# Optimization experiments

Measured on AMD Instinct MI355X. Metric: run time of the kernel, lower is better.

Reference implementation:

```python
import math
import jax, jax.numpy as jnp
import numpy as np

PROB_SPARSE_FACTOR = 0.4


def setup_inputs() -> dict:
    key = jax.random.key(0)
    kq, kk, kv = jax.random.split(key, 3)
    B, H, T, S, D = 2, 16, 2048, 2048, 64
    q = jax.random.normal(kq, (B, H, T, D), dtype=jnp.float32)
    k = jax.random.normal(kk, (B, H, S, D), dtype=jnp.float32)
    v = jax.random.normal(kv, (B, H, S, D), dtype=jnp.float32)
    return {"q": q, "k": k, "v": v}


def reference(q, k, v):
    B, H, T, D = q.shape
    S = k.shape[2]
    scaling = 1.0 / math.sqrt(D)
    # Informer-style top-u query count (static, derived from shapes)
    u = max(int(min(PROB_SPARSE_FACTOR * math.log(S), T * 0.5)), int(T * 0.3))

    # KLD scoring over full attention approximation: [B,H,T,S]
    attn_approx = jnp.einsum("bhtd,bhsd->bhts", q * scaling, k)
    attn_approx = jnp.clip(attn_approx, -50.0, 50.0)
    attn_approx = attn_approx - jnp.max(attn_approx, axis=-1, keepdims=True)
    sm = jax.nn.softmax(attn_approx, axis=-1)
    log_uniform = math.log(S)
    kl_score = jnp.sum(sm * (jnp.log(sm + 1e-10) + log_uniform), axis=-1)  # [B,H,T]

    # Select top-u most informative queries per (b,h)
    _, topk_idx = jax.lax.top_k(kl_score, u)  # [B,H,u]

    # Sparse attention only for selected queries
    q_red = jnp.take_along_axis(q, topk_idx[..., None], axis=2)  # [B,H,u,D]
    scores = jnp.einsum("bhud,bhsd->bhus", q_red, k) * scaling
    scores = jnp.clip(scores, -50.0, 50.0)
    scores = scores - jnp.max(scores, axis=-1, keepdims=True)
    w = jax.nn.softmax(scores, axis=-1)
    w = jnp.clip(w, 1e-9, 1.0)
    out_red = jnp.einsum("bhus,bhsd->bhud", w, v)  # [B,H,u,D]

    # Scatter reduced outputs back into a zero-initialized full output
    b_i = jnp.arange(B)[:, None, None]
    h_i = jnp.arange(H)[None, :, None]
    out = jnp.zeros_like(q).at[b_i, h_i, topk_idx].set(out_red)
    return out
```

## Files before the change

### kernel.cpp

```cpp
#include <hip/hip_runtime.h>
#include <math.h>

#define T_DIM 2048
#define S_DIM 2048
#define D_DIM 64
#define BH_DIM 32
#define U_SEL 614
#define LOG_S_D 7.624618986159398
#define LOG2E_F 1.4426950408889634f
#define LN2_D 0.6931471805599453
#define SCL_Q (0.125f * LOG2E_F)

typedef __attribute__((ext_vector_type(8))) short bf16x8;
typedef __attribute__((ext_vector_type(4))) short bf16x4;
typedef __attribute__((ext_vector_type(4))) float f32x4;

__device__ __forceinline__ unsigned short bf16_rne(float x) {
  unsigned u = __float_as_uint(x);
  u += 0x7FFF + ((u >> 16) & 1);
  return (unsigned short)(u >> 16);
}
__device__ __forceinline__ float bf16_to_f(unsigned short h) {
  return __uint_as_float(((unsigned)h) << 16);
}

#define GLD_LDS16(g, l)                                                        \
  __builtin_amdgcn_global_load_lds(                                            \
      (const __attribute__((address_space(1))) unsigned int*)(const void*)(g), \
      (__attribute__((address_space(3))) unsigned int*)(void*)(l), 16, 0, 0)

__device__ __forceinline__ void stage_img(const unsigned short* __restrict__ g,
                                          unsigned short* l, int lane, int w) {
#pragma unroll
  for (int it = 0; it < 4; ++it) {
    const int chunk = it * 4 + w;
    GLD_LDS16((const char*)g + chunk * 1024 + lane * 16, (char*)l + chunk * 1024);
  }
}

__device__ __forceinline__ bf16x8 ldfrag_sw(const unsigned short* buf, int row, int chunk) {
  return *(const bf16x8*)(buf + (row << 6) + (((chunk) ^ (row & 7)) << 3));
}

__global__ __launch_bounds__(256) void convert_kernel(
    const float* __restrict__ kin, const float* __restrict__ vin,
    unsigned short* __restrict__ khi_g, unsigned short* __restrict__ klo_g,
    unsigned short* __restrict__ vt_g, float* __restrict__ out) {
  __shared__ float vld[128][65];
  const int jb = blockIdx.x;
  const int tid = threadIdx.x;
  if (jb < 512) {
    const int bh = jb >> 4, tl = jb & 15;
    const float* src = kin + ((size_t)bh * 2048 + tl * 128) * 64;
    unsigned short* dhi = khi_g + (size_t)(bh * 16 + tl) * 8192;
    unsigned short* dlo = klo_g + (size_t)(bh * 16 + tl) * 8192;
#pragma unroll
    for (int g = 0; g < 4; ++g) {
      const int flat = g * 256 + tid;
      const int r = flat >> 3, c = flat & 7;
      const float4 f0 = *(const float4*)(src + r * 64 + c * 8);
      const float4 f1 = *(const float4*)(src + r * 64 + c * 8 + 4);
      const float xs[8] = {f0.x, f0.y, f0.z, f0.w, f1.x, f1.y, f1.z, f1.w};
      bf16x8 hv, lv;
#pragma unroll
      for (int j = 0; j < 8; ++j) {
        const unsigned short h = bf16_rne(xs[j]);
        hv[j] = (short)h;
        lv[j] = (short)bf16_rne(xs[j] - bf16_to_f(h));
      }
      const int base = (r << 6) + ((c ^ (r & 7)) << 3);
      *(bf16x8*)(dhi + base) = hv;
      *(bf16x8*)(dlo + base) = lv;
    }
  } else if (jb < 1024) {
    const int jv = jb - 512;
    const int bh = jv >> 4, tl = jv & 15;
    const float* src = vin + ((size_t)bh * 2048 + tl * 128) * 64;
#pragma unroll
    for (int g = 0; g < 8; ++g) {
      const int f = g * 256 + tid;
      const int r = f >> 4, c4 = f & 15;
      const float4 x = *(const float4*)(src + r * 64 + c4 * 4);
      vld[r][c4 * 4 + 0] = x.x;
      vld[r][c4 * 4 + 1] = x.y;
      vld[r][c4 * 4 + 2] = x.z;
      vld[r][c4 * 4 + 3] = x.w;
    }
    __syncthreads();
    unsigned short* dst = vt_g + (size_t)(bh * 16 + tl) * 8192;
#pragma unroll
    for (int g = 0; g < 4; ++g) {
      const int oc = g * 256 + tid;
      const int d = oc >> 4, cc = oc & 15;
      bf16x8 hv;
#pragma unroll
      for (int j = 0; j < 8; ++j) hv[j] = (short)bf16_rne(vld[cc * 8 + j][d]);
      *(bf16x8*)(dst + (d << 7) + (((cc ^ (d & 15))) << 3)) = hv;
    }
  } else {
    float4* o4 = (float4*)out;
    const size_t b = (size_t)(jb - 1024);
#pragma unroll
    for (int g = 0; g < 8; ++g)
      o4[b * 2048 + g * 256 + tid] = make_float4(0.f, 0.f, 0.f, 0.f);
  }
}

__global__ __launch_bounds__(256, 2) void kl_score_mfma(
    const float* __restrict__ q, const unsigned short* __restrict__ khi_g,
    const unsigned short* __restrict__ klo_g, float* __restrict__ klout) {
  __shared__ __align__(16) unsigned short lds[2][16384];
  const int bh = blockIdx.y;
  const int t0 = blockIdx.x * 128;
  const int tid = threadIdx.x;
  const int lane = tid & 63, w = tid >> 6, quad = lane >> 4, l15 = lane & 15;
  const float* qb = q + (size_t)bh * (2048 * 64) + (size_t)t0 * 64;
  const unsigned short* khb = khi_g + (size_t)bh * 16 * 8192;
  const unsigned short* klb = klo_g + (size_t)bh * 16 * 8192;

  {
    unsigned short* qhi = &lds[1][0];
    unsigned short* qlo = &lds[1][8192];
#pragma unroll
    for (int g = 0; g < 4; ++g) {
      const int flat = g * 256 + tid;
      const int r = flat >> 3, c = flat & 7;
      const float4 f0 = *(const float4*)(qb + r * 64 + c * 8);
      const float4 f1 = *(const float4*)(qb + r * 64 + c * 8 + 4);
      const float xs[8] = {f0.x, f0.y, f0.z, f0.w, f1.x, f1.y, f1.z, f1.w};
      bf16x8 hv, lv;
#pragma unroll
      for (int j = 0; j < 8; ++j) {
        const float x = xs[j] * SCL_Q;
        const unsigned short h = bf16_rne(x);
        hv[j] = (short)h;
        lv[j] = (short)bf16_rne(x - bf16_to_f(h));
      }
      const int base = (r << 6) + ((c ^ (r & 7)) << 3);
      *(bf16x8*)(qhi + base) = hv;
      *(bf16x8*)(qlo + base) = lv;
    }
  }
  stage_img(khb, &lds[0][0], lane, w);
  stage_img(klb, &lds[0][8192], lane, w);
  __syncthreads();

  bf16x8 ah[2][2], al[2][2];
#pragma unroll
  for (int rt = 0; rt < 2; ++rt) {
    const int row = w * 32 + rt * 16 + l15;
#pragma unroll
    for (int kc = 0; kc < 2; ++kc) {
      ah[rt][kc] = ldfrag_sw(&lds[1][0], row, kc * 4 + quad);
      al[rt][kc] = ldfrag_sw(&lds[1][8192], row, kc * 4 + quad);
    }
  }
  __syncthreads();

  double Zd[8], Wd[8];
#pragma unroll
  for (int i = 0; i < 8; ++i) { Zd[i] = 0.0; Wd[i] = 0.0; }

  for (int st = 0; st < 16; ++st) {
    if (st < 15) {
      unsigned short* nb = &lds[(st + 1) & 1][0];
      stage_img(khb + (size_t)(st + 1) * 8192, nb, lane, w);
      stage_img(klb + (size_t)(st + 1) * 8192, nb + 8192, lane, w);
    }
    const unsigned short* cb = &lds[st & 1][0];

    f32x4 acc[2][8];
#pragma unroll
    for (int rt = 0; rt < 2; ++rt)
#pragma unroll
      for (int ct = 0; ct < 8; ++ct) acc[rt][ct] = (f32x4){0.f, 0.f, 0.f, 0.f};

#pragma unroll
    for (int ct = 0; ct < 8; ++ct) {
      const int srow = ct * 16 + l15;
      const bf16x8 bh0 = ldfrag_sw(cb, srow, quad);
      const bf16x8 bl0 = ldfrag_sw(cb + 8192, srow, quad);
      const bf16x8 bh1 = ldfrag_sw(cb, srow, 4 + quad);
      const bf16x8 bl1 = ldfrag_sw(cb + 8192, srow, 4 + quad);
#pragma unroll
      for (int rt = 0; rt < 2; ++rt) {
        f32x4 c = acc[rt][ct];
        c = __builtin_amdgcn_mfma_f32_16x16x32_bf16(ah[rt][0], bh0, c, 0, 0, 0);
        c = __builtin_amdgcn_mfma_f32_16x16x32_bf16(al[rt][0], bh0, c, 0, 0, 0);
        c = __builtin_amdgcn_mfma_f32_16x16x32_bf16(ah[rt][0], bl0, c, 0, 0, 0);
        c = __builtin_amdgcn_mfma_f32_16x16x32_bf16(ah[rt][1], bh1, c, 0, 0, 0);
        c = __builtin_amdgcn_mfma_f32_16x16x32_bf16(al[rt][1], bh1, c, 0, 0, 0);
        c = __builtin_amdgcn_mfma_f32_16x16x32_bf16(ah[rt][1], bl1, c, 0, 0, 0);
        acc[rt][ct] = c;
      }
    }

#pragma unroll
    for (int rt = 0; rt < 2; ++rt)
#pragma unroll
      for (int r = 0; r < 4; ++r) {
        float zp = 0.f, wp = 0.f;
#pragma unroll
        for (int ct = 0; ct < 8; ++ct) {
          const float t = acc[rt][ct][r];
          const float e = exp2f(t);
          zp += e;
          wp = fmaf(e, t, wp);
        }
        Zd[rt * 4 + r] += (double)zp;
        Wd[rt * 4 + r] += (double)wp;
      }
    __syncthreads();
  }

#pragma unroll
  for (int i = 0; i < 8; ++i) {
    double Zt = Zd[i], Wt = Wd[i];
#pragma unroll
    for (int mask = 1; mask <= 8; mask <<= 1) {
      Zt += __shfl_xor(Zt, mask);
      Wt += __shfl_xor(Wt, mask);
    }
    if (l15 == 0) {
      const double kl = LN2_D * (Wt / Zt) - log(Zt) + LOG_S_D;
      const int row = t0 + w * 32 + (i >> 2) * 16 + quad * 4 + (i & 3);
      klout[(size_t)bh * T_DIM + row] = (float)kl;
    }
  }
}

__global__ __launch_bounds__(1024) void topk_kernel(const float* __restrict__ kl,
                                                    int* __restrict__ topk) {
  __shared__ float sv[2048];
  __shared__ int si[2048];
  const int bh = blockIdx.x;
  const int tid = threadIdx.x;
  for (int i = tid; i < 2048; i += 1024) { sv[i] = kl[(size_t)bh * 2048 + i]; si[i] = i; }
  __syncthreads();
  for (int kk = 2; kk <= 2048; kk <<= 1) {
    for (int j = kk >> 1; j > 0; j >>= 1) {
      const int p = tid;
      const int i = ((p & ~(j - 1)) << 1) | (p & (j - 1));
      const int pr = i | j;
      const float v1 = sv[i], v2 = sv[pr];
      const int i1 = si[i], i2 = si[pr];
      const bool beforePI = (v2 > v1) || (v2 == v1 && i2 < i1);
      const bool dirDesc = ((i & kk) == 0);
      const bool doSwap = dirDesc ? beforePI : !beforePI;
      if (doSwap) { sv[i] = v2; sv[pr] = v1; si[i] = i2; si[pr] = i1; }
      __syncthreads();
    }
  }
  for (int i = tid; i < U_SEL; i += 1024) topk[bh * U_SEL + i] = si[i];
}

struct __align__(16) SmC {
  unsigned short qs[64 * 64];
  unsigned short kt[128 * 64];
  union { unsigned short vt[64 * 128]; float obuf[64 * 64]; } u;
  unsigned short ps[4][64 * 40];
  float zred[4][64];
};

__global__ __launch_bounds__(256, 2) void sparse_attn_mfma(
    const float* __restrict__ q, const unsigned short* __restrict__ khi_g,
    const unsigned short* __restrict__ vt_g, const int* __restrict__ topk,
    float* __restrict__ out) {
  __shared__ SmC sm;
  const int bh = blockIdx.y;
  const int l0 = blockIdx.x * 64;
  const int tid = threadIdx.x;
  const int lane = tid & 63, w = tid >> 6, quad = lane >> 4, l15 = lane & 15;
  const float* qb = q + (size_t)bh * (2048 * 64);
  const unsigned short* khb = khi_g + (size_t)bh * 16 * 8192;
  const unsigned short* vtb = vt_g + (size_t)bh * 16 * 8192;
  const int* tkb = topk + bh * U_SEL;

  {
#pragma unroll
    for (int g = 0; g < 2; ++g) {
      const int ch = g * 256 + tid;
      const int r = ch >> 3, c = ch & 7;
      const int l = l0 + r;
      const int row = (l < U_SEL) ? tkb[l] : tkb[0];
      const float4 f0 = *(const float4*)(qb + (size_t)row * 64 + c * 8);
      const float4 f1 = *(const float4*)(qb + (size_t)row * 64 + c * 8 + 4);
      const float xs[8] = {f0.x, f0.y, f0.z, f0.w, f1.x, f1.y, f1.z, f1.w};
      bf16x8 hv;
#pragma unroll
      for (int j = 0; j < 8; ++j) hv[j] = (short)bf16_rne(xs[j] * SCL_Q);
      *(bf16x8*)&sm.qs[(r << 6) + ((c ^ (r & 7)) << 3)] = hv;
    }
  }
  stage_img(khb, sm.kt, lane, w);
  stage_img(vtb, sm.u.vt, lane, w);
  __syncthreads();

  bf16x8 qf[4][2];
#pragma unroll
  for (int nt = 0; nt < 4; ++nt)
#pragma unroll
    for (int kc = 0; kc < 2; ++kc)
      qf[nt][kc] = ldfrag_sw(sm.qs, nt * 16 + l15, kc * 4 + quad);

  float zrun[4] = {0.f, 0.f, 0.f, 0.f};
  f32x4 oacc[4][4];
#pragma unroll
  for (int a = 0; a < 4; ++a)
#pragma unroll
    for (int b = 0; b < 4; ++b) oacc[a][b] = (f32x4){0.f, 0.f, 0.f, 0.f};

  for (int st = 0; st < 16; ++st) {
    f32x4 sacc[2][4];
#pragma unroll
    for (int mt = 0; mt < 2; ++mt)
#pragma unroll
      for (int nt = 0; nt < 4; ++nt) sacc[mt][nt] = (f32x4){0.f, 0.f, 0.f, 0.f};
#pragma unroll
    for (int mt = 0; mt < 2; ++mt) {
      const int arow = w * 32 + mt * 16 + l15;
      const bf16x8 a0 = ldfrag_sw(sm.kt, arow, quad);
      const bf16x8 a1 = ldfrag_sw(sm.kt, arow, 4 + quad);
#pragma unroll
      for (int nt = 0; nt < 4; ++nt) {
        f32x4 c = sacc[mt][nt];
        c = __builtin_amdgcn_mfma_f32_16x16x32_bf16(a0, qf[nt][0], c, 0, 0, 0);
        c = __builtin_amdgcn_mfma_f32_16x16x32_bf16(a1, qf[nt][1], c, 0, 0, 0);
        sacc[mt][nt] = c;
      }
    }

#pragma unroll
    for (int nt = 0; nt < 4; ++nt) {
      float zl = 0.f;
#pragma unroll
      for (int mt = 0; mt < 2; ++mt) {
        bf16x4 pw;
#pragma unroll
        for (int r = 0; r < 4; ++r) {
          const float p = exp2f(sacc[mt][nt][r]);
          zl += p;
          pw[r] = (short)bf16_rne(p);
        }
        *(bf16x4*)&sm.ps[w][(nt * 16 + l15) * 40 + mt * 16 + quad * 4] = pw;
      }
      zrun[nt] += zl;
    }

    {
      bf16x8 vbf[4];
#pragma unroll
      for (int dt = 0; dt < 4; ++dt) {
        const int d = dt * 16 + l15;
        vbf[dt] = *(const bf16x8*)&sm.u.vt[(d << 7) + (((w * 4 + quad) ^ l15) << 3)];
      }
#pragma unroll
      for (int mtq = 0; mtq < 4; ++mtq) {
        const bf16x8 pa = *(const bf16x8*)&sm.ps[w][(mtq * 16 + l15) * 40 + quad * 8];
#pragma unroll
        for (int dt = 0; dt < 4; ++dt)
          oacc[mtq][dt] = __builtin_amdgcn_mfma_f32_16x16x32_bf16(pa, vbf[dt], oacc[mtq][dt], 0, 0, 0);
      }
    }
    __syncthreads();
    if (st < 15) {
      stage_img(khb + (size_t)(st + 1) * 8192, sm.kt, lane, w);
      stage_img(vtb + (size_t)(st + 1) * 8192, sm.u.vt, lane, w);
      __syncthreads();
    }
  }

#pragma unroll
  for (int nt = 0; nt < 4; ++nt) {
    float z = zrun[nt];
    z += __shfl_xor(z, 16);
    z += __shfl_xor(z, 32);
    if (quad == 0) sm.zred[w][nt * 16 + l15] = z;
  }
  for (int i = tid; i < 64 * 64; i += 256) sm.u.obuf[i] = 0.f;
  __syncthreads();
#pragma unroll
  for (int mtq = 0; mtq < 4; ++mtq)
#pragma unroll
    for (int r = 0; r < 4; ++r) {
      const int qr = mtq * 16 + quad * 4 + r;
#pragma unroll
      for (int dt = 0; dt < 4; ++dt)
        atomicAdd(&sm.u.obuf[qr * 64 + dt * 16 + l15], oacc[mtq][dt][r]);
    }
  __syncthreads();
  {
    const int qr = tid >> 2, seg = tid & 3;
    const int l = l0 + qr;
    if (l < U_SEL) {
      const float Zt = sm.zred[0][qr] + sm.zred[1][qr] + sm.zred[2][qr] + sm.zred[3][qr];
      const float inv = 1.0f / Zt;
      const int row = tkb[l];
      float* op = &out[((size_t)bh * T_DIM + row) * 64 + seg * 16];
      const float* ob = &sm.u.obuf[qr * 64 + seg * 16];
#pragma unroll
      for (int j = 0; j < 4; ++j) {
        float4 o;
        o.x = ob[j * 4 + 0] * inv;
        o.y = ob[j * 4 + 1] * inv;
        o.z = ob[j * 4 + 2] * inv;
        o.w = ob[j * 4 + 3] * inv;
        *(float4*)&op[j * 4] = o;
      }
    }
  }
}

extern "C" void kernel_launch(void* const* d_in, const int* in_sizes, int n_in,
                              void* d_out, int out_size, void* d_ws, size_t ws_size,
                              hipStream_t stream) {
  const float* q = (const float*)d_in[0];
  const float* k = (const float*)d_in[1];
  const float* v = (const float*)d_in[2];
  float* out = (float*)d_out;
  char* ws = (char*)d_ws;
  float* kl = (float*)ws;
  int* topk = (int*)(ws + 262144);
  unsigned short* khi_g = (unsigned short*)(ws + 524288);
  unsigned short* klo_g = (unsigned short*)(ws + 8912896);
  unsigned short* vt_g = (unsigned short*)(ws + 17301504);

  convert_kernel<<<dim3(1536), dim3(256), 0, stream>>>(k, v, khi_g, klo_g, vt_g, out);
  kl_score_mfma<<<dim3(T_DIM / 128, BH_DIM), dim3(256), 0, stream>>>(q, khi_g, klo_g, kl);
  topk_kernel<<<dim3(BH_DIM), dim3(1024), 0, stream>>>(kl, topk);
  sparse_attn_mfma<<<dim3((U_SEL + 63) / 64, BH_DIM), dim3(256), 0, stream>>>(q, khi_g, vt_g, topk, out);
}
```

Before: 254.7 us.

## Split KL scoring over key halves with interleaved K hi/lo tiles and float partials

```diff
diff --git a/kernel.cpp b/kernel.cpp
--- a/kernel.cpp
+++ b/kernel.cpp
@@ -29,33 +29,44 @@
       (const __attribute__((address_space(1))) unsigned int*)(const void*)(g), \
       (__attribute__((address_space(3))) unsigned int*)(void*)(l), 16, 0, 0)
 
-__device__ __forceinline__ void stage_img(const unsigned short* __restrict__ g,
-                                          unsigned short* l, int lane, int w) {
+__device__ __forceinline__ void stage_img16(const unsigned short* __restrict__ g,
+                                            unsigned short* l, int lane, int w) {
 #pragma unroll
   for (int it = 0; it < 4; ++it) {
     const int chunk = it * 4 + w;
     GLD_LDS16((const char*)g + chunk * 1024 + lane * 16, (char*)l + chunk * 1024);
   }
 }
+__device__ __forceinline__ void stage_img8(const unsigned short* __restrict__ g,
+                                           unsigned short* l, int lane, int w) {
+#pragma unroll
+  for (int it = 0; it < 2; ++it) {
+    const int chunk = it * 4 + w;
+    GLD_LDS16((const char*)g + chunk * 1024 + lane * 16, (char*)l + chunk * 1024);
+  }
+}
 
 __device__ __forceinline__ bf16x8 ldfrag_sw(const unsigned short* buf, int row, int chunk) {
   return *(const bf16x8*)(buf + (row << 6) + (((chunk) ^ (row & 7)) << 3));
 }
+__device__ __forceinline__ bf16x8 ldfrag_k128(const unsigned short* buf, int row, int chunk) {
+  return *(const bf16x8*)(buf + ((row >> 6) << 12) + ((row & 63) << 6) +
+                          (((chunk) ^ (row & 7)) << 3));
+}
 
 __global__ __launch_bounds__(256) void convert_kernel(
     const float* __restrict__ kin, const float* __restrict__ vin,
-    unsigned short* __restrict__ khi_g, unsigned short* __restrict__ klo_g,
-    unsigned short* __restrict__ vt_g, float* __restrict__ out) {
+    unsigned short* __restrict__ kimg, unsigned short* __restrict__ vt_g,
+    float* __restrict__ out) {
   __shared__ float vld[128][65];
   const int jb = blockIdx.x;
   const int tid = threadIdx.x;
-  if (jb < 512) {
-    const int bh = jb >> 4, tl = jb & 15;
-    const float* src = kin + ((size_t)bh * 2048 + tl * 128) * 64;
-    unsigned short* dhi = khi_g + (size_t)(bh * 16 + tl) * 8192;
-    unsigned short* dlo = klo_g + (size_t)(bh * 16 + tl) * 8192;
-#pragma unroll
-    for (int g = 0; g < 4; ++g) {
+  if (jb < 1024) {
+    const int bh = jb >> 5, tl = jb & 31;
+    const float* src = kin + ((size_t)bh * 2048 + tl * 64) * 64;
+    unsigned short* dst = kimg + (size_t)(bh * 32 + tl) * 8192;
+#pragma unroll
+    for (int g = 0; g < 2; ++g) {
       const int flat = g * 256 + tid;
       const int r = flat >> 3, c = flat & 7;
       const float4 f0 = *(const float4*)(src + r * 64 + c * 8);
@@ -69,11 +80,11 @@
         lv[j] = (short)bf16_rne(xs[j] - bf16_to_f(h));
       }
       const int base = (r << 6) + ((c ^ (r & 7)) << 3);
-      *(bf16x8*)(dhi + base) = hv;
-      *(bf16x8*)(dlo + base) = lv;
-    }
-  } else if (jb < 1024) {
-    const int jv = jb - 512;
+      *(bf16x8*)(dst + base) = hv;
+      *(bf16x8*)(dst + 4096 + base) = lv;
+    }
+  } else if (jb < 1536) {
+    const int jv = jb - 1024;
     const int bh = jv >> 4, tl = jv & 15;
     const float* src = vin + ((size_t)bh * 2048 + tl * 128) * 64;
 #pragma unroll
@@ -99,28 +110,28 @@
     }
   } else {
     float4* o4 = (float4*)out;
-    const size_t b = (size_t)(jb - 1024);
+    const size_t b = (size_t)(jb - 1536);
 #pragma unroll
     for (int g = 0; g < 8; ++g)
       o4[b * 2048 + g * 256 + tid] = make_float4(0.f, 0.f, 0.f, 0.f);
   }
 }
 
-__global__ __launch_bounds__(256, 2) void kl_score_mfma(
-    const float* __restrict__ q, const unsigned short* __restrict__ khi_g,
-    const unsigned short* __restrict__ klo_g, float* __restrict__ klout) {
-  __shared__ __align__(16) unsigned short lds[2][16384];
-  const int bh = blockIdx.y;
-  const int t0 = blockIdx.x * 128;
+__global__ __launch_bounds__(256, 4) void kl_score_mfma(
+    const float* __restrict__ q, const unsigned short* __restrict__ kimg,
+    float2* __restrict__ zw) {
+  __shared__ __align__(16) unsigned short lbuf[2][8192];
+  const int b = blockIdx.x;
+  const int bh = b & 31;
+  const int t0 = ((b >> 5) & 15) * 128;
+  const int shalf = b >> 9;
   const int tid = threadIdx.x;
   const int lane = tid & 63, w = tid >> 6, quad = lane >> 4, l15 = lane & 15;
   const float* qb = q + (size_t)bh * (2048 * 64) + (size_t)t0 * 64;
-  const unsigned short* khb = khi_g + (size_t)bh * 16 * 8192;
-  const unsigned short* klb = klo_g + (size_t)bh * 16 * 8192;
+  const unsigned short* kb = kimg + (size_t)bh * (32 * 8192);
+  const int tg0 = shalf * 16;
 
   {
-    unsigned short* qhi = &lds[1][0];
-    unsigned short* qlo = &lds[1][8192];
 #pragma unroll
     for (int g = 0; g < 4; ++g) {
       const int flat = g * 256 + tid;
@@ -136,13 +147,12 @@
         hv[j] = (short)h;
         lv[j] = (short)bf16_rne(x - bf16_to_f(h));
       }
-      const int base = (r << 6) + ((c ^ (r & 7)) << 3);
-      *(bf16x8*)(qhi + base) = hv;
-      *(bf16x8*)(qlo + base) = lv;
-    }
-  }
-  stage_img(khb, &lds[0][0], lane, w);
-  stage_img(klb, &lds[0][8192], lane, w);
+      const int r2 = r & 63, hi2 = r >> 6;
+      const int base = hi2 * 4096 + (r2 << 6) + ((c ^ (r2 & 7)) << 3);
+      *(bf16x8*)(&lbuf[0][0] + base) = hv;
+      *(bf16x8*)(&lbuf[1][0] + base) = lv;
+    }
+  }
   __syncthreads();
 
   bf16x8 ah[2][2], al[2][2];
@@ -151,37 +161,37 @@
     const int row = w * 32 + rt * 16 + l15;
 #pragma unroll
     for (int kc = 0; kc < 2; ++kc) {
-      ah[rt][kc] = ldfrag_sw(&lds[1][0], row, kc * 4 + quad);
-      al[rt][kc] = ldfrag_sw(&lds[1][8192], row, kc * 4 + quad);
-    }
-  }
-  __syncthreads();
-
-  double Zd[8], Wd[8];
-#pragma unroll
-  for (int i = 0; i < 8; ++i) { Zd[i] = 0.0; Wd[i] = 0.0; }
-
-  for (int st = 0; st < 16; ++st) {
-    if (st < 15) {
-      unsigned short* nb = &lds[(st + 1) & 1][0];
-      stage_img(khb + (size_t)(st + 1) * 8192, nb, lane, w);
-      stage_img(klb + (size_t)(st + 1) * 8192, nb + 8192, lane, w);
-    }
-    const unsigned short* cb = &lds[st & 1][0];
-
-    f32x4 acc[2][8];
+      ah[rt][kc] = ldfrag_k128(&lbuf[0][0], row, kc * 4 + quad);
+      al[rt][kc] = ldfrag_k128(&lbuf[1][0], row, kc * 4 + quad);
+    }
+  }
+  __syncthreads();
+
+  stage_img16(kb + (size_t)tg0 * 8192, &lbuf[0][0], lane, w);
+  __syncthreads();
+
+  float Zf[8], Wf[8];
+#pragma unroll
+  for (int i = 0; i < 8; ++i) { Zf[i] = 0.f; Wf[i] = 0.f; }
+
+  for (int t = 0; t < 16; ++t) {
+    if (t < 15)
+      stage_img16(kb + (size_t)(tg0 + t + 1) * 8192, &lbuf[(t + 1) & 1][0], lane, w);
+    const unsigned short* cb = &lbuf[t & 1][0];
+
+    f32x4 acc[2][4];
 #pragma unroll
     for (int rt = 0; rt < 2; ++rt)
 #pragma unroll
-      for (int ct = 0; ct < 8; ++ct) acc[rt][ct] = (f32x4){0.f, 0.f, 0.f, 0.f};
-
-#pragma unroll
-    for (int ct = 0; ct < 8; ++ct) {
+      for (int ct = 0; ct < 4; ++ct) acc[rt][ct] = (f32x4){0.f, 0.f, 0.f, 0.f};
+
+#pragma unroll
+    for (int ct = 0; ct < 4; ++ct) {
       const int srow = ct * 16 + l15;
       const bf16x8 bh0 = ldfrag_sw(cb, srow, quad);
-      const bf16x8 bl0 = ldfrag_sw(cb + 8192, srow, quad);
+      const bf16x8 bl0 = ldfrag_sw(cb + 4096, srow, quad);
       const bf16x8 bh1 = ldfrag_sw(cb, srow, 4 + quad);
-      const bf16x8 bl1 = ldfrag_sw(cb + 8192, srow, 4 + quad);
+      const bf16x8 bl1 = ldfrag_sw(cb + 4096, srow, 4 + quad);
 #pragma unroll
       for (int rt = 0; rt < 2; ++rt) {
         f32x4 c = acc[rt][ct];
@@ -201,41 +211,47 @@
       for (int r = 0; r < 4; ++r) {
         float zp = 0.f, wp = 0.f;
 #pragma unroll
-        for (int ct = 0; ct < 8; ++ct) {
-          const float t = acc[rt][ct][r];
-          const float e = exp2f(t);
+        for (int ct = 0; ct < 4; ++ct) {
+          const float tt = acc[rt][ct][r];
+          const float e = exp2f(tt);
           zp += e;
-          wp = fmaf(e, t, wp);
+          wp = fmaf(e, tt, wp);
         }
-        Zd[rt * 4 + r] += (double)zp;
-        Wd[rt * 4 + r] += (double)wp;
+        Zf[rt * 4 + r] += zp;
+        Wf[rt * 4 + r] += wp;
       }
     __syncthreads();
   }
 
 #pragma unroll
   for (int i = 0; i < 8; ++i) {
-    double Zt = Zd[i], Wt = Wd[i];
+    float Zt = Zf[i], Wt = Wf[i];
 #pragma unroll
     for (int mask = 1; mask <= 8; mask <<= 1) {
       Zt += __shfl_xor(Zt, mask);
       Wt += __shfl_xor(Wt, mask);
     }
     if (l15 == 0) {
-      const double kl = LN2_D * (Wt / Zt) - log(Zt) + LOG_S_D;
       const int row = t0 + w * 32 + (i >> 2) * 16 + quad * 4 + (i & 3);
-      klout[(size_t)bh * T_DIM + row] = (float)kl;
-    }
-  }
-}
-
-__global__ __launch_bounds__(1024) void topk_kernel(const float* __restrict__ kl,
+      zw[((size_t)shalf * 32 + bh) * 2048 + row] = make_float2(Zt, Wt);
+    }
+  }
+}
+
+__global__ __launch_bounds__(1024) void topk_kernel(const float2* __restrict__ zw,
                                                     int* __restrict__ topk) {
   __shared__ float sv[2048];
   __shared__ int si[2048];
   const int bh = blockIdx.x;
   const int tid = threadIdx.x;
-  for (int i = tid; i < 2048; i += 1024) { sv[i] = kl[(size_t)bh * 2048 + i]; si[i] = i; }
+  for (int i = tid; i < 2048; i += 1024) {
+    const float2 a = zw[(size_t)bh * 2048 + i];
+    const float2 c = zw[(size_t)(32 + bh) * 2048 + i];
+    const double Z = (double)a.x + (double)c.x;
+    const double W = (double)a.y + (double)c.y;
+    sv[i] = (float)(LN2_D * (W / Z) - log(Z) + LOG_S_D);
+    si[i] = i;
+  }
   __syncthreads();
   for (int kk = 2; kk <= 2048; kk <<= 1) {
     for (int j = kk >> 1; j > 0; j >>= 1) {
@@ -262,18 +278,19 @@
   float zred[4][64];
 };
 
-__global__ __launch_bounds__(256, 2) void sparse_attn_mfma(
-    const float* __restrict__ q, const unsigned short* __restrict__ khi_g,
+__global__ __launch_bounds__(256, 3) void sparse_attn_mfma(
+    const float* __restrict__ q, const unsigned short* __restrict__ kimg,
     const unsigned short* __restrict__ vt_g, const int* __restrict__ topk,
     float* __restrict__ out) {
   __shared__ SmC sm;
-  const int bh = blockIdx.y;
-  const int l0 = blockIdx.x * 64;
+  const int b = blockIdx.x;
+  const int bh = b & 31;
+  const int l0 = (b >> 5) * 64;
   const int tid = threadIdx.x;
   const int lane = tid & 63, w = tid >> 6, quad = lane >> 4, l15 = lane & 15;
   const float* qb = q + (size_t)bh * (2048 * 64);
-  const unsigned short* khb = khi_g + (size_t)bh * 16 * 8192;
-  const unsigned short* vtb = vt_g + (size_t)bh * 16 * 8192;
+  const unsigned short* kb = kimg + (size_t)bh * (32 * 8192);
+  const unsigned short* vtb = vt_g + (size_t)bh * (16 * 8192);
   const int* tkb = topk + bh * U_SEL;
 
   {
@@ -292,8 +309,9 @@
       *(bf16x8*)&sm.qs[(r << 6) + ((c ^ (r & 7)) << 3)] = hv;
     }
   }
-  stage_img(khb, sm.kt, lane, w);
-  stage_img(vtb, sm.u.vt, lane, w);
+  stage_img8(kb, sm.kt, lane, w);
+  stage_img8(kb + 8192, sm.kt + 4096, lane, w);
+  stage_img16(vtb, sm.u.vt, lane, w);
   __syncthreads();
 
   bf16x8 qf[4][2];
@@ -308,7 +326,7 @@
 #pragma unroll
   for (int a = 0; a < 4; ++a)
 #pragma unroll
-    for (int b = 0; b < 4; ++b) oacc[a][b] = (f32x4){0.f, 0.f, 0.f, 0.f};
+    for (int b2 = 0; b2 < 4; ++b2) oacc[a][b2] = (f32x4){0.f, 0.f, 0.f, 0.f};
 
   for (int st = 0; st < 16; ++st) {
     f32x4 sacc[2][4];
@@ -319,8 +337,8 @@
 #pragma unroll
     for (int mt = 0; mt < 2; ++mt) {
       const int arow = w * 32 + mt * 16 + l15;
-      const bf16x8 a0 = ldfrag_sw(sm.kt, arow, quad);
-      const bf16x8 a1 = ldfrag_sw(sm.kt, arow, 4 + quad);
+      const bf16x8 a0 = ldfrag_k128(sm.kt, arow, quad);
+      const bf16x8 a1 = ldfrag_k128(sm.kt, arow, 4 + quad);
 #pragma unroll
       for (int nt = 0; nt < 4; ++nt) {
         f32x4 c = sacc[mt][nt];
@@ -364,8 +382,9 @@
     }
     __syncthreads();
     if (st < 15) {
-      stage_img(khb + (size_t)(st + 1) * 8192, sm.kt, lane, w);
-      stage_img(vtb + (size_t)(st + 1) * 8192, sm.u.vt, lane, w);
+      stage_img8(kb + (size_t)(2 * st + 2) * 8192, sm.kt, lane, w);
+      stage_img8(kb + (size_t)(2 * st + 3) * 8192, sm.kt + 4096, lane, w);
+      stage_img16(vtb + (size_t)(st + 1) * 8192, sm.u.vt, lane, w);
       __syncthreads();
     }
   }
@@ -419,14 +438,13 @@
   const float* v = (const float*)d_in[2];
   float* out = (float*)d_out;
   char* ws = (char*)d_ws;
-  float* kl = (float*)ws;
-  int* topk = (int*)(ws + 262144);
-  unsigned short* khi_g = (unsigned short*)(ws + 524288);
-  unsigned short* klo_g = (unsigned short*)(ws + 8912896);
-  unsigned short* vt_g = (unsigned short*)(ws + 17301504);
-
-  convert_kernel<<<dim3(1536), dim3(256), 0, stream>>>(k, v, khi_g, klo_g, vt_g, out);
-  kl_score_mfma<<<dim3(T_DIM / 128, BH_DIM), dim3(256), 0, stream>>>(q, khi_g, klo_g, kl);
-  topk_kernel<<<dim3(BH_DIM), dim3(1024), 0, stream>>>(kl, topk);
-  sparse_attn_mfma<<<dim3((U_SEL + 63) / 64, BH_DIM), dim3(256), 0, stream>>>(q, khi_g, vt_g, topk, out);
-}
+  float2* zw = (float2*)ws;
+  int* topk = (int*)(ws + 1048576);
+  unsigned short* kimg = (unsigned short*)(ws + 1310720);
+  unsigned short* vt_g = (unsigned short*)(ws + 18087936);
+
+  convert_kernel<<<dim3(2048), dim3(256), 0, stream>>>(k, v, kimg, vt_g, out);
+  kl_score_mfma<<<dim3(1024), dim3(256), 0, stream>>>(q, kimg, zw);
+  topk_kernel<<<dim3(BH_DIM), dim3(1024), 0, stream>>>(zw, topk);
+  sparse_attn_mfma<<<dim3(320), dim3(256), 0, stream>>>(q, kimg, vt_g, topk, out);
+}
```

New measurement: 251.2 us. Within noise of the previous version (-1.4%).
